# Optimization experiments

Measured on AMD Instinct MI355X. Metric: run time of the kernel, lower is better.

Reference implementation:

```python
import jax, jax.numpy as jnp
import numpy as np

B, S, H, L = 64, 2048, 1024, 15


def setup_inputs() -> dict:
    key = jax.random.key(0)
    ks = jax.random.split(key, 16)
    x = jax.random.normal(ks[0], (B, S, H), dtype=jnp.float32)
    # valid spans: start in [1, S-40), length in [1, 32)
    s1 = jax.random.randint(ks[1], (B,), 1, S - 40)
    l1 = jax.random.randint(ks[2], (B,), 1, 32)
    s2 = jax.random.randint(ks[3], (B,), 1, S - 40)
    l2 = jax.random.randint(ks[4], (B,), 1, 32)
    entity_idx = jnp.stack([s1, s1 + l1, s2, s2 + l2], axis=1).astype(jnp.int32)
    sc = 1.0 / np.sqrt(H)
    W_cls = jax.random.normal(ks[5], (H, H), jnp.float32) * sc
    b_cls = jnp.zeros((H,), jnp.float32)
    W_e1 = jax.random.normal(ks[6], (H, H), jnp.float32) * sc
    b_e1 = jnp.zeros((H,), jnp.float32)
    W_e2 = jax.random.normal(ks[7], (H, H), jnp.float32) * sc
    b_e2 = jnp.zeros((H,), jnp.float32)
    W1 = jax.random.normal(ks[8], (3 * H, H), jnp.float32) * (1.0 / np.sqrt(3 * H))
    b1 = jnp.zeros((H,), jnp.float32)
    W2 = jax.random.normal(ks[9], (H, H), jnp.float32) * sc
    b2 = jnp.zeros((H,), jnp.float32)
    Wout = jax.random.normal(ks[10], (H, L), jnp.float32) * sc
    bout = jnp.zeros((L,), jnp.float32)
    return {"x": x, "entity_idx": entity_idx, "W_cls": W_cls, "b_cls": b_cls,
            "W_e1": W_e1, "b_e1": b_e1, "W_e2": W_e2, "b_e2": b_e2,
            "W1": W1, "b1": b1, "W2": W2, "b2": b2, "Wout": Wout, "bout": bout}


def _span_mean(x, start, end):
    # x: [B,S,H]; start,end: [B] int -> masked mean over [start,end)
    pos = jnp.arange(x.shape[1])[None, :]  # [1,S]
    mask = ((pos >= start[:, None]) & (pos < end[:, None])).astype(x.dtype)  # [B,S]
    cnt = jnp.maximum(mask.sum(axis=1, keepdims=True), 1.0)  # [B,1]
    return jnp.einsum('bs,bsh->bh', mask, x) / cnt


def reference(x, entity_idx, W_cls, b_cls, W_e1, b_e1, W_e2, b_e2,
              W1, b1, W2, b2, Wout, bout):
    subj = _span_mean(x, entity_idx[:, 0], entity_idx[:, 1])  # [B,H]
    obj = _span_mean(x, entity_idx[:, 2], entity_idx[:, 3])   # [B,H]
    x0 = jnp.tanh(x[:, 0, :]) @ W_cls + b_cls
    e1 = jnp.tanh(subj) @ W_e1 + b_e1
    e2 = jnp.tanh(obj) @ W_e2 + b_e2
    h = jnp.concatenate([x0, e1, e2], axis=1)  # [B,3H]
    h = h @ W1 + b1           # dropout is identity at eval
    h = h @ W2 + b2
    out = h @ Wout + bout     # [B,num_labels]
    return out
```

## Files before the change

kernel.cpp:

```cpp
#include <hip/hip_runtime.h>
#include <math.h>

#define BB 64
#define SS 2048
#define HH 1024
#define LL 15

__global__ void span_tanh_kernel(const float* __restrict__ x,
                                 const int* __restrict__ eidx,
                                 float* __restrict__ t_cat) {
  int b = blockIdx.x;
  int tid = threadIdx.x;
  int s1 = eidx[b * 4 + 0], e1 = eidx[b * 4 + 1];
  int s2 = eidx[b * 4 + 2], e2 = eidx[b * 4 + 3];
  float c1 = (float)max(e1 - s1, 1);
  float c2 = (float)max(e2 - s2, 1);
  const float* xb = x + (size_t)b * SS * HH;
  float* tb = t_cat + (size_t)b * 3 * HH;
  for (int h = tid; h < HH; h += 256) {
    float v0 = xb[h];
    float a1 = 0.f, a2 = 0.f;
    for (int s = s1; s < e1; ++s) a1 += xb[(size_t)s * HH + h];
    for (int s = s2; s < e2; ++s) a2 += xb[(size_t)s * HH + h];
    tb[h]          = tanhf(v0);
    tb[HH + h]     = tanhf(a1 / c1);
    tb[2 * HH + h] = tanhf(a2 / c2);
  }
}

__device__ __forceinline__ void gemm_tile_body(
    const float* __restrict__ A, int lda,
    const float* __restrict__ W, int ldw,
    const float* __restrict__ bias,
    float* __restrict__ C, int ldc,
    int k0, int kend, int j0, bool addBias, bool useAtomic) {
  __shared__ float As[64][33];
  __shared__ float Ws[32][64];
  int tid = threadIdx.x;
  int tx = tid & 15, ty = tid >> 4;
  float acc[4][4] = {{0.f}};
  for (int kb = k0; kb < kend; kb += 32) {
#pragma unroll
    for (int i = 0; i < 8; ++i) {
      int idx = tid + i * 256;
      As[idx >> 5][idx & 31] = A[(size_t)(idx >> 5) * lda + kb + (idx & 31)];
    }
#pragma unroll
    for (int i = 0; i < 8; ++i) {
      int idx = tid + i * 256;
      Ws[idx >> 6][idx & 63] = W[(size_t)(kb + (idx >> 6)) * ldw + j0 + (idx & 63)];
    }
    __syncthreads();
#pragma unroll
    for (int kk = 0; kk < 32; ++kk) {
      float a[4], w[4];
#pragma unroll
      for (int i = 0; i < 4; ++i) a[i] = As[ty * 4 + i][kk];
#pragma unroll
      for (int j = 0; j < 4; ++j) w[j] = Ws[kk][tx * 4 + j];
#pragma unroll
      for (int i = 0; i < 4; ++i)
#pragma unroll
        for (int j = 0; j < 4; ++j) acc[i][j] += a[i] * w[j];
    }
    __syncthreads();
  }
#pragma unroll
  for (int i = 0; i < 4; ++i) {
    int r = ty * 4 + i;
#pragma unroll
    for (int j = 0; j < 4; ++j) {
      int c = j0 + tx * 4 + j;
      float v = acc[i][j];
      if (addBias) v += bias[c];
      if (useAtomic) atomicAdd(&C[(size_t)r * ldc + c], v);
      else C[(size_t)r * ldc + c] = v;
    }
  }
}

__global__ void gemm_bd_kernel(const float* __restrict__ t_cat,
                               const float* __restrict__ Wc, const float* __restrict__ bc,
                               const float* __restrict__ We1, const float* __restrict__ be1,
                               const float* __restrict__ We2, const float* __restrict__ be2,
                               float* __restrict__ h_cat, int Kchunk) {
  int z = blockIdx.z;
  const float* W = (z == 0) ? Wc : ((z == 1) ? We1 : We2);
  const float* bias = (z == 0) ? bc : ((z == 1) ? be1 : be2);
  const float* A = t_cat + z * HH;
  float* C = h_cat + z * HH;
  int k0 = blockIdx.y * Kchunk;
  gemm_tile_body(A, 3 * HH, W, HH, bias, C, 3 * HH,
                 k0, k0 + Kchunk, blockIdx.x * 64,
                 blockIdx.y == 0, true);
}

__global__ void gemm_kernel(const float* __restrict__ A, int lda,
                            const float* __restrict__ W, int ldw,
                            const float* __restrict__ bias,
                            float* __restrict__ C, int ldc, int Kchunk) {
  int k0 = blockIdx.y * Kchunk;
  gemm_tile_body(A, lda, W, ldw, bias, C, ldc,
                 k0, k0 + Kchunk, blockIdx.x * 64,
                 blockIdx.y == 0, gridDim.y > 1);
}

__global__ void out_kernel(const float* __restrict__ h2,
                           const float* __restrict__ Wout,
                           const float* __restrict__ bout,
                           float* __restrict__ out) {
  int idx = blockIdx.x * blockDim.x + threadIdx.x;
  if (idx >= BB * LL) return;
  int b = idx / LL, l = idx % LL;
  const float* h = h2 + (size_t)b * HH;
  float acc = bout[l];
#pragma unroll 8
  for (int k = 0; k < HH; ++k) acc += h[k] * Wout[(size_t)k * LL + l];
  out[idx] = acc;
}

extern "C" void kernel_launch(void* const* d_in, const int* in_sizes, int n_in,
                              void* d_out, int out_size, void* d_ws, size_t ws_size,
                              hipStream_t stream) {
  const float* x     = (const float*)d_in[0];
  const int*   eidx  = (const int*)d_in[1];
  const float* W_cls = (const float*)d_in[2];
  const float* b_cls = (const float*)d_in[3];
  const float* W_e1  = (const float*)d_in[4];
  const float* b_e1  = (const float*)d_in[5];
  const float* W_e2  = (const float*)d_in[6];
  const float* b_e2  = (const float*)d_in[7];
  const float* W1    = (const float*)d_in[8];
  const float* b1    = (const float*)d_in[9];
  const float* W2    = (const float*)d_in[10];
  const float* b2    = (const float*)d_in[11];
  const float* Wout  = (const float*)d_in[12];
  const float* bout  = (const float*)d_in[13];
  float* out = (float*)d_out;

  float* ws    = (float*)d_ws;
  float* t_cat = ws;
  float* h_cat = t_cat + BB * 3 * HH;
  float* h1    = h_cat + BB * 3 * HH;
  float* h2    = h1 + BB * HH;

  hipMemsetAsync(h_cat, 0, (size_t)(BB * 3 * HH + BB * HH + BB * HH) * sizeof(float), stream);

  span_tanh_kernel<<<BB, 256, 0, stream>>>(x, eidx, t_cat);

  gemm_bd_kernel<<<dim3(16, 4, 3), 256, 0, stream>>>(
      t_cat, W_cls, b_cls, W_e1, b_e1, W_e2, b_e2, h_cat, 256);

  gemm_kernel<<<dim3(16, 8, 1), 256, 0, stream>>>(h_cat, 3 * HH, W1, HH, b1, h1, HH, 384);

  gemm_kernel<<<dim3(16, 4, 1), 256, 0, stream>>>(h1, HH, W2, HH, b2, h2, HH, 256);

  out_kernel<<<dim3((BB * LL + 255) / 256), 256, 0, stream>>>(h2, Wout, bout, out);
}
```

Measured before the change: 827.8 us.

## Register-prefetch vectorized GEMM tiles, fuse zeroing into span kernel, parallelize output GEMV

```diff
diff --git a/kernel.cpp b/kernel.cpp
--- a/kernel.cpp
+++ b/kernel.cpp
@@ -8,56 +8,85 @@
 
 __global__ void span_tanh_kernel(const float* __restrict__ x,
                                  const int* __restrict__ eidx,
-                                 float* __restrict__ t_cat) {
+                                 float* __restrict__ t_cat,
+                                 float* __restrict__ h_cat,
+                                 float* __restrict__ h1,
+                                 float* __restrict__ h2) {
   int b = blockIdx.x;
+  int hc = blockIdx.y;
   int tid = threadIdx.x;
+  int h = hc * 256 + tid;
+
+  {
+    float* z = h_cat + (size_t)b * 3 * HH + hc * 768;
+    for (int i = tid; i < 768; i += 256) z[i] = 0.f;
+    h1[(size_t)b * HH + hc * 256 + tid] = 0.f;
+    h2[(size_t)b * HH + hc * 256 + tid] = 0.f;
+  }
+
   int s1 = eidx[b * 4 + 0], e1 = eidx[b * 4 + 1];
   int s2 = eidx[b * 4 + 2], e2 = eidx[b * 4 + 3];
   float c1 = (float)max(e1 - s1, 1);
   float c2 = (float)max(e2 - s2, 1);
   const float* xb = x + (size_t)b * SS * HH;
   float* tb = t_cat + (size_t)b * 3 * HH;
-  for (int h = tid; h < HH; h += 256) {
-    float v0 = xb[h];
-    float a1 = 0.f, a2 = 0.f;
-    for (int s = s1; s < e1; ++s) a1 += xb[(size_t)s * HH + h];
-    for (int s = s2; s < e2; ++s) a2 += xb[(size_t)s * HH + h];
-    tb[h]          = tanhf(v0);
-    tb[HH + h]     = tanhf(a1 / c1);
-    tb[2 * HH + h] = tanhf(a2 / c2);
-  }
+
+  float v0 = xb[h];
+  float a1 = 0.f, a2 = 0.f;
+  for (int s = s1; s < e1; ++s) a1 += xb[(size_t)s * HH + h];
+  for (int s = s2; s < e2; ++s) a2 += xb[(size_t)s * HH + h];
+  tb[h]          = tanhf(v0);
+  tb[HH + h]     = tanhf(a1 / c1);
+  tb[2 * HH + h] = tanhf(a2 / c2);
 }
 
+#define LSTR 68
 __device__ __forceinline__ void gemm_tile_body(
     const float* __restrict__ A, int lda,
     const float* __restrict__ W, int ldw,
     const float* __restrict__ bias,
     float* __restrict__ C, int ldc,
-    int k0, int kend, int j0, bool addBias, bool useAtomic) {
-  __shared__ float As[64][33];
-  __shared__ float Ws[32][64];
+    int k0, int kend, int j0, bool addBias) {
+  __shared__ float As[32 * LSTR];
+  __shared__ float Ws[32 * LSTR];
   int tid = threadIdx.x;
   int tx = tid & 15, ty = tid >> 4;
+
+  float4 aReg[2], wReg[2];
+  int aRow[2], aKq[2], wRow[2], wCq[2];
+#pragma unroll
+  for (int i = 0; i < 2; ++i) {
+    int idx = tid + i * 256;
+    aRow[i] = idx & 63; aKq[i] = idx >> 6;
+    wRow[i] = idx >> 4; wCq[i] = idx & 15;
+  }
+
+  auto loadRegs = [&](int kb) {
+#pragma unroll
+    for (int i = 0; i < 2; ++i) {
+      aReg[i] = *(const float4*)&A[(size_t)aRow[i] * lda + kb + 4 * aKq[i]];
+      wReg[i] = *(const float4*)&W[(size_t)(kb + wRow[i]) * ldw + j0 + 4 * wCq[i]];
+    }
+  };
+
   float acc[4][4] = {{0.f}};
+  loadRegs(k0);
   for (int kb = k0; kb < kend; kb += 32) {
 #pragma unroll
-    for (int i = 0; i < 8; ++i) {
-      int idx = tid + i * 256;
-      As[idx >> 5][idx & 31] = A[(size_t)(idx >> 5) * lda + kb + (idx & 31)];
-    }
+    for (int i = 0; i < 2; ++i) {
+      float av[4] = {aReg[i].x, aReg[i].y, aReg[i].z, aReg[i].w};
 #pragma unroll
-    for (int i = 0; i < 8; ++i) {
-      int idx = tid + i * 256;
-      Ws[idx >> 6][idx & 63] = W[(size_t)(kb + (idx >> 6)) * ldw + j0 + (idx & 63)];
+      for (int j = 0; j < 4; ++j) As[(4 * aKq[i] + j) * LSTR + aRow[i]] = av[j];
+      *(float4*)&Ws[wRow[i] * LSTR + 4 * wCq[i]] = wReg[i];
     }
     __syncthreads();
+    if (kb + 32 < kend) loadRegs(kb + 32);
 #pragma unroll
     for (int kk = 0; kk < 32; ++kk) {
-      float a[4], w[4];
-#pragma unroll
-      for (int i = 0; i < 4; ++i) a[i] = As[ty * 4 + i][kk];
-#pragma unroll
-      for (int j = 0; j < 4; ++j) w[j] = Ws[kk][tx * 4 + j];
+      float4 a4 = *(const float4*)&As[kk * LSTR + ty * 4];
+      float4 w4 = *(const float4*)&Ws[kk * LSTR + tx * 4];
+      float a[4] = {a4.x, a4.y, a4.z, a4.w};
+      float w[4] = {w4.x, w4.y, w4.z, w4.w};
 #pragma unroll
       for (int i = 0; i < 4; ++i)
 #pragma unroll
@@ -73,8 +102,7 @@
       int c = j0 + tx * 4 + j;
       float v = acc[i][j];
       if (addBias) v += bias[c];
-      if (useAtomic) atomicAdd(&C[(size_t)r * ldc + c], v);
-      else C[(size_t)r * ldc + c] = v;
+      atomicAdd(&C[(size_t)r * ldc + c], v);
     }
   }
 }
@@ -91,8 +119,7 @@
   float* C = h_cat + z * HH;
   int k0 = blockIdx.y * Kchunk;
   gemm_tile_body(A, 3 * HH, W, HH, bias, C, 3 * HH,
-                 k0, k0 + Kchunk, blockIdx.x * 64,
-                 blockIdx.y == 0, true);
+                 k0, k0 + Kchunk, blockIdx.x * 64, blockIdx.y == 0);
 }
 
 __global__ void gemm_kernel(const float* __restrict__ A, int lda,
@@ -101,22 +128,31 @@
                             float* __restrict__ C, int ldc, int Kchunk) {
   int k0 = blockIdx.y * Kchunk;
   gemm_tile_body(A, lda, W, ldw, bias, C, ldc,
-                 k0, k0 + Kchunk, blockIdx.x * 64,
-                 blockIdx.y == 0, gridDim.y > 1);
+                 k0, k0 + Kchunk, blockIdx.x * 64, blockIdx.y == 0);
 }
 
 __global__ void out_kernel(const float* __restrict__ h2,
                            const float* __restrict__ Wout,
                            const float* __restrict__ bout,
                            float* __restrict__ out) {
-  int idx = blockIdx.x * blockDim.x + threadIdx.x;
-  if (idx >= BB * LL) return;
+  int tid = threadIdx.x;
+  int lane = tid & 63;
+  int idx = blockIdx.x * 4 + (tid >> 6);
   int b = idx / LL, l = idx % LL;
   const float* h = h2 + (size_t)b * HH;
-  float acc = bout[l];
-#pragma unroll 8
-  for (int k = 0; k < HH; ++k) acc += h[k] * Wout[(size_t)k * LL + l];
-  out[idx] = acc;
+  float acc = 0.f;
+#pragma unroll
+  for (int w = 0; w < 4; ++w) {
+    int k0 = (w * 64 + lane) * 4;
+    float4 h4 = *(const float4*)&h[k0];
+    acc += h4.x * Wout[(size_t)(k0 + 0) * LL + l];
+    acc += h4.y * Wout[(size_t)(k0 + 1) * LL + l];
+    acc += h4.z * Wout[(size_t)(k0 + 2) * LL + l];
+    acc += h4.w * Wout[(size_t)(k0 + 3) * LL + l];
+  }
+#pragma unroll
+  for (int off = 32; off > 0; off >>= 1) acc += __shfl_down(acc, off, 64);
+  if (lane == 0) out[idx] = acc + bout[l];
 }
 
 extern "C" void kernel_launch(void* const* d_in, const int* in_sizes, int n_in,
@@ -144,16 +180,14 @@
   float* h1    = h_cat + BB * 3 * HH;
   float* h2    = h1 + BB * HH;
 
-  hipMemsetAsync(h_cat, 0, (size_t)(BB * 3 * HH + BB * HH + BB * HH) * sizeof(float), stream);
-
-  span_tanh_kernel<<<BB, 256, 0, stream>>>(x, eidx, t_cat);
+  span_tanh_kernel<<<dim3(BB, 4), 256, 0, stream>>>(x, eidx, t_cat, h_cat, h1, h2);
 
   gemm_bd_kernel<<<dim3(16, 4, 3), 256, 0, stream>>>(
       t_cat, W_cls, b_cls, W_e1, b_e1, W_e2, b_e2, h_cat, 256);
 
-  gemm_kernel<<<dim3(16, 8, 1), 256, 0, stream>>>(h_cat, 3 * HH, W1, HH, b1, h1, HH, 384);
+  gemm_kernel<<<dim3(16, 12, 1), 256, 0, stream>>>(h_cat, 3 * HH, W1, HH, b1, h1, HH, 256);
 
-  gemm_kernel<<<dim3(16, 4, 1), 256, 0, stream>>>(h1, HH, W2, HH, b2, h2, HH, 256);
+  gemm_kernel<<<dim3(16, 8, 1), 256, 0, stream>>>(h1, HH, W2, HH, b2, h2, HH, 128);
 
-  out_kernel<<<dim3((BB * LL + 255) / 256), 256, 0, stream>>>(h2, Wout, bout, out);
+  out_kernel<<<dim3(240), 256, 0, stream>>>(h2, Wout, bout, out);
 }
```

Result: faster. 726.4 us (-12.2%).
